# Kernel tuning notes

Hardware: AMD Instinct MI355X
Metric: run time of the kernel (lower is better)

## Reference

```python
import jax, jax.numpy as jnp
import numpy as np

NUM_BOXES = 512
NUM_COORDS = 200000
C = 128
MAX_SELECTED = 262144  # static pad size for the ragged output
P_INSIDE = 0.002       # expected ~204.8k selected rows < MAX_SELECTED


def setup_inputs() -> dict:
    key = jax.random.key(0)
    k1, k2, k3 = jax.random.split(key, 3)
    coords = jax.random.randint(k1, (NUM_COORDS, 4), 0, 256, dtype=jnp.int32)
    features = jax.random.normal(k2, (NUM_COORDS, C), dtype=jnp.float32)
    is_inside = jax.random.uniform(k3, (NUM_BOXES, NUM_COORDS)) < P_INSIDE
    return {"coords": coords, "features": features, "is_inside": is_inside,
            "max_selected": MAX_SELECTED}


def reference(coords, features, is_inside, max_selected):
    # Faithful to select_coords/select_features, but WITHOUT materializing the
    # dense (num_boxes, num_coords, C) expand: compute flat nonzero indices of
    # the mask directly and gather once. Output is padded to a static size
    # (padded rows zeroed) since jax requires static shapes.
    num_boxes, num_coords = is_inside.shape
    total = num_boxes * num_coords
    flat_idx = jnp.nonzero(is_inside.ravel(), size=max_selected, fill_value=total)[0]
    valid = flat_idx < total                      # [K] pad mask
    safe = jnp.where(valid, flat_idx, 0)
    box_idx = (safe // num_coords).astype(jnp.int32)   # [K]
    coord_idx = safe % num_coords                       # [K]
    # select_features: features[None].expand(...)[is_inside]
    selected_features = jnp.where(valid[:, None], features[coord_idx], 0.0)  # [K, C]
    # select_coords: cat(coords[:, :-1] gathered, box index)
    sel_xyz = coords[coord_idx, :-1]                    # [K, 3]
    ext_coords = jnp.concatenate([sel_xyz, box_idx[:, None]], axis=-1)  # [K, 4]
    extended_coordinates = jnp.where(valid[:, None], ext_coords, 0)
    return extended_coordinates, selected_features
```

## Files before the change

### kernel.cpp

```cpp
#include <hip/hip_runtime.h>


#define BS  256
#define WPB 1024
#define DETB 32

__device__ __forceinline__ unsigned nzmask4(unsigned v){
  unsigned t = (v | ((v & 0x7f7f7f7fu) + 0x7f7f7f7fu)) & 0x80808080u;
  return ((t >> 7) & 1u) | ((t >> 14) & 2u) | ((t >> 21) & 4u) | ((t >> 28) & 8u);
}
__device__ __forceinline__ unsigned nzmask16(uint4 x){
  return nzmask4(x.x) | (nzmask4(x.y) << 4) | (nzmask4(x.z) << 8) | (nzmask4(x.w) << 12);
}

__global__ void detect_mode(const uchar4* p, int nvec, int* flags){
  int found = 0;
  for (int i = blockIdx.x*blockDim.x + threadIdx.x; i < nvec;
       i += gridDim.x*blockDim.x){
    uchar4 v = p[i];
    if (v.y) found = 1;
  }
  __shared__ int sh;
  if (threadIdx.x == 0) sh = 0;
  __syncthreads();
  if (found) atomicOr(&sh, 1);
  __syncthreads();
  if (threadIdx.x == 0) flags[blockIdx.x] = sh;
}

__global__ void pack_count(const void* data, const int* flags,
                           long long totalElems, int wordsTotal,
                           unsigned* maskOut, int* counts){
  __shared__ int modeSh;
  if (threadIdx.x == 0){
    int f = 0;
    for (int i = 0; i < DETB; ++i) f |= flags[i];
    modeSh = f;
  }
  __syncthreads();
  const bool byteMode = (modeSh != 0);
  const int tid = threadIdx.x;
  int cnt = 0;
  const int wBase = blockIdx.x * WPB;
  if (byteMode){
    const uint4* d = (const uint4*)data;
    const unsigned char* p8 = (const unsigned char*)data;
    for (int i = tid; i < WPB; i += BS){
      const int w = wBase + i;
      if (w >= wordsTotal) break;
      const long long e0 = (long long)w << 5;
      unsigned m;
      if (e0 + 31 < totalElems){
        uint4 a = d[2*w], b = d[2*w+1];
        m = nzmask16(a) | (nzmask16(b) << 16);
      } else {
        m = 0;
        for (int b = 0; b < 32 && e0 + b < totalElems; ++b)
          if (p8[e0 + b]) m |= (1u << b);
      }
      maskOut[w] = m;
      cnt += __popc(m);
    }
  } else {
    const uint4* d = (const uint4*)data;
    const unsigned* p32 = (const unsigned*)data;
    for (int i = tid; i < WPB; i += BS){
      const int w = wBase + i;
      if (w >= wordsTotal) break;
      const long long e0 = (long long)w << 5;
      unsigned m = 0;
      if (e0 + 31 < totalElems){
        #pragma unroll
        for (int k = 0; k < 8; ++k){
          uint4 x = d[8*(long long)w + k];
          m |= ((unsigned)(x.x!=0) << (4*k)) | ((unsigned)(x.y!=0) << (4*k+1)) |
               ((unsigned)(x.z!=0) << (4*k+2)) | ((unsigned)(x.w!=0) << (4*k+3));
        }
      } else {
        for (int b = 0; b < 32 && e0 + b < totalElems; ++b)
          if (p32[e0 + b]) m |= (1u << b);
      }
      maskOut[w] = m;
      cnt += __popc(m);
    }
  }
  const int lane = tid & 63, wid = tid >> 6;
  for (int off = 32; off > 0; off >>= 1) cnt += __shfl_down(cnt, off, 64);
  __shared__ int wsum[BS/64];
  if (lane == 0) wsum[wid] = cnt;
  __syncthreads();
  if (tid == 0){
    int s = 0;
    for (int w = 0; w < BS/64; ++w) s += wsum[w];
    counts[blockIdx.x] = s;
  }
}

__global__ void scan_kernel(const int* counts, int* offsets, int* totalOut, int nb){
  const int tid = threadIdx.x;
  const int per = (nb + BS - 1)/BS;
  const int base = tid*per;
  int vals[16];
  int sum = 0;
  for (int k = 0; k < per; ++k){
    int idx = base + k;
    int c = (idx < nb) ? counts[idx] : 0;
    vals[k] = sum; sum += c;
  }
  int incl = sum;
  const int lane = tid & 63, wid = tid >> 6;
  for (int off = 1; off < 64; off <<= 1){
    int t = __shfl_up(incl, off, 64);
    if (lane >= off) incl += t;
  }
  __shared__ int wsum[BS/64];
  if (lane == 63) wsum[wid] = incl;
  __syncthreads();
  int wbase = 0;
  for (int w = 0; w < wid; ++w) wbase += wsum[w];
  const int excl = wbase + incl - sum;
  for (int k = 0; k < per; ++k){
    int idx = base + k;
    if (idx < nb) offsets[idx] = excl + vals[k];
  }
  if (tid == BS-1){
    int t = 0;
    for (int w = 0; w < BS/64; ++w) t += wsum[w];
    *totalOut = t;
  }
}

__global__ void emit_kernel(const unsigned* mask, const int* offsets,
                            int wordsTotal, int max_sel, int* outIdx){
  const int tid = threadIdx.x;
  const int lane = tid & 63, wid = tid >> 6;
  const int wBase = blockIdx.x * WPB;
  int running = offsets[blockIdx.x];
  __shared__ int wsum[BS/64];
  const int iters = WPB / BS;
  for (int it = 0; it < iters; ++it){
    const int w = wBase + it*BS + tid;
    unsigned m = (w < wordsTotal) ? mask[w] : 0u;
    const int cnt = __popc(m);
    int incl = cnt;
    for (int off = 1; off < 64; off <<= 1){
      int t = __shfl_up(incl, off, 64);
      if (lane >= off) incl += t;
    }
    if (lane == 63) wsum[wid] = incl;
    __syncthreads();
    int wbase = 0;
    for (int ww = 0; ww < wid; ++ww) wbase += wsum[ww];
    int iterTotal = 0;
    for (int ww = 0; ww < BS/64; ++ww) iterTotal += wsum[ww];
    int pos = running + wbase + incl - cnt;
    if (m){
      const long long e0 = (long long)w << 5;
      unsigned mm = m;
      while (mm){
        const int b = __ffs(mm) - 1;
        mm &= mm - 1;
        if (pos < max_sel) outIdx[pos] = (int)(e0 + b);
        ++pos;
      }
    }
    running += iterTotal;
    __syncthreads();
  }
}

__global__ void gather_kernel(const int* selIdx, const int* totalPtr,
                              const int4* coords, const float4* feat,
                              int num_coords, int c4, int max_sel,
                              float4* outExt, float4* outFeat){
  const int lane = threadIdx.x & 31;
  const int rowsPerBlock = blockDim.x >> 5;
  const int r = blockIdx.x*rowsPerBlock + (threadIdx.x >> 5);
  if (r >= max_sel) return;
  int total = *totalPtr;
  if (total > max_sel) total = max_sel;
  if (r < total){
    const int flat = selIdx[r];
    const unsigned box = (unsigned)flat / (unsigned)num_coords;
    const int ci = flat - (int)box*num_coords;
    const float4* src = feat + (long long)ci*c4;
    float4* dst = outFeat + (long long)r*c4;
    for (int c = lane; c < c4; c += 32) dst[c] = src[c];
    if (lane == 0){
      int4 cc = coords[ci];
      outExt[r] = make_float4((float)cc.x, (float)cc.y, (float)cc.z, (float)box);
    }
  } else {
    const float4 z = make_float4(0.f, 0.f, 0.f, 0.f);
    float4* dst = outFeat + (long long)r*c4;
    for (int c = lane; c < c4; c += 32) dst[c] = z;
    if (lane == 0) outExt[r] = z;
  }
}

extern "C" void kernel_launch(void* const* d_in, const int* in_sizes, int n_in,
                              void* d_out, int out_size, void* d_ws, size_t ws_size,
                              hipStream_t stream){
  const int*   coords   = (const int*)d_in[0];
  const float* features = (const float*)d_in[1];
  const void*  inside   = d_in[2];

  const int num_coords = in_sizes[0] / 4;
  const int C          = in_sizes[1] / num_coords;
  const int c4         = C / 4;
  const long long totalElems = (long long)in_sizes[2];
  const int max_sel    = out_size / (4 + C);

  const int wordsTotal = (int)((totalElems + 31) / 32);
  const int NBP        = (wordsTotal + WPB - 1) / WPB;

  int* ws      = (int*)d_ws;
  int* flags   = ws;
  int* total   = ws + DETB;
  int* counts  = ws + DETB + 1;
  int* offsets = counts + NBP;
  int* selIdx  = offsets + NBP;
  unsigned* maskBuf = (unsigned*)(selIdx + max_sel);

  hipLaunchKernelGGL(detect_mode, dim3(DETB), dim3(BS), 0, stream,
                     (const uchar4*)inside, 65536 , flags);
  hipLaunchKernelGGL(pack_count, dim3(NBP), dim3(BS), 0, stream,
                     inside, flags, totalElems, wordsTotal, maskBuf, counts);
  hipLaunchKernelGGL(scan_kernel, dim3(1), dim3(BS), 0, stream,
                     counts, offsets, total, NBP);
  hipLaunchKernelGGL(emit_kernel, dim3(NBP), dim3(BS), 0, stream,
                     maskBuf, offsets, wordsTotal, max_sel, selIdx);
  const int rowsPerBlock = BS / 32;
  const int gblocks = (max_sel + rowsPerBlock - 1) / rowsPerBlock;
  hipLaunchKernelGGL(gather_kernel, dim3(gblocks), dim3(BS), 0, stream,
                     selIdx, total, (const int4*)coords, (const float4*)features,
                     num_coords, c4, max_sel,
                     (float4*)d_out,
                     (float4*)((float*)d_out + (long long)max_sel*4));
}
```

Measured before the change: 670.9 us.

## Make pack/emit per-wavefront chunks, add nontemporal loads/stores, grid-stride gather

Pack and emit kernels now give each 64-lane wavefront its own chunk of mask words, which removes the block-level shared-memory reductions and __syncthreads. Mask reads and gather output writes use nontemporal loads and stores to avoid polluting cache during streaming. The gather kernel becomes a fixed 2048-block grid-stride loop. The scan now handles four times more chunk counts (vals array raised to 64), so the single-block scan does more serial work per thread.

```diff
diff --git a/kernel.cpp b/kernel.cpp
--- a/kernel.cpp
+++ b/kernel.cpp
@@ -1,15 +1,20 @@
 #include <hip/hip_runtime.h>
 
 
-#define BS  256
-#define WPB 1024
+#define BS   256
+#define WPW  256
+#define CPB  4
 #define DETB 32
+
+using uint4v  = __attribute__((ext_vector_type(4))) unsigned int;
+using int4v   = __attribute__((ext_vector_type(4))) int;
+using float4v = __attribute__((ext_vector_type(4))) float;
 
 __device__ __forceinline__ unsigned nzmask4(unsigned v){
   unsigned t = (v | ((v & 0x7f7f7f7fu) + 0x7f7f7f7fu)) & 0x80808080u;
   return ((t >> 7) & 1u) | ((t >> 14) & 2u) | ((t >> 21) & 4u) | ((t >> 28) & 8u);
 }
-__device__ __forceinline__ unsigned nzmask16(uint4 x){
+__device__ __forceinline__ unsigned nzmask16(uint4v x){
   return nzmask4(x.x) | (nzmask4(x.y) << 4) | (nzmask4(x.z) << 8) | (nzmask4(x.w) << 12);
 }
 
@@ -29,7 +34,7 @@
 }
 
 __global__ void pack_count(const void* data, const int* flags,
-                           long long totalElems, int wordsTotal,
+                           long long totalElems, int wordsTotal, int nchunks,
                            unsigned* maskOut, int* counts){
   __shared__ int modeSh;
   if (threadIdx.x == 0){
@@ -39,68 +44,66 @@
   }
   __syncthreads();
   const bool byteMode = (modeSh != 0);
-  const int tid = threadIdx.x;
+  const int lane  = threadIdx.x & 63;
+  const int wv    = threadIdx.x >> 6;
+  const int chunk = blockIdx.x*CPB + wv;
+  if (chunk >= nchunks) return;
+  const int wBase = chunk * WPW;
   int cnt = 0;
-  const int wBase = blockIdx.x * WPB;
   if (byteMode){
-    const uint4* d = (const uint4*)data;
+    const uint4v* d = (const uint4v*)data;
     const unsigned char* p8 = (const unsigned char*)data;
-    for (int i = tid; i < WPB; i += BS){
-      const int w = wBase + i;
-      if (w >= wordsTotal) break;
+    #pragma unroll
+    for (int it = 0; it < WPW/64; ++it){
+      const int w = wBase + it*64 + lane;
+      if (w >= wordsTotal) continue;
       const long long e0 = (long long)w << 5;
       unsigned m;
       if (e0 + 31 < totalElems){
-        uint4 a = d[2*w], b = d[2*w+1];
+        uint4v a = __builtin_nontemporal_load(d + 2*(long long)w);
+        uint4v b = __builtin_nontemporal_load(d + 2*(long long)w + 1);
         m = nzmask16(a) | (nzmask16(b) << 16);
       } else {
         m = 0;
-        for (int b = 0; b < 32 && e0 + b < totalElems; ++b)
-          if (p8[e0 + b]) m |= (1u << b);
+        for (int bb = 0; bb < 32 && e0 + bb < totalElems; ++bb)
+          if (p8[e0 + bb]) m |= (1u << bb);
       }
       maskOut[w] = m;
       cnt += __popc(m);
     }
   } else {
-    const uint4* d = (const uint4*)data;
+    const uint4v* d = (const uint4v*)data;
     const unsigned* p32 = (const unsigned*)data;
-    for (int i = tid; i < WPB; i += BS){
-      const int w = wBase + i;
-      if (w >= wordsTotal) break;
+    #pragma unroll
+    for (int it = 0; it < WPW/64; ++it){
+      const int w = wBase + it*64 + lane;
+      if (w >= wordsTotal) continue;
       const long long e0 = (long long)w << 5;
       unsigned m = 0;
       if (e0 + 31 < totalElems){
         #pragma unroll
         for (int k = 0; k < 8; ++k){
-          uint4 x = d[8*(long long)w + k];
-          m |= ((unsigned)(x.x!=0) << (4*k)) | ((unsigned)(x.y!=0) << (4*k+1)) |
+          uint4v x = __builtin_nontemporal_load(d + 8*(long long)w + k);
+          m |= ((unsigned)(x.x!=0) << (4*k))   | ((unsigned)(x.y!=0) << (4*k+1)) |
                ((unsigned)(x.z!=0) << (4*k+2)) | ((unsigned)(x.w!=0) << (4*k+3));
         }
       } else {
-        for (int b = 0; b < 32 && e0 + b < totalElems; ++b)
-          if (p32[e0 + b]) m |= (1u << b);
+        for (int bb = 0; bb < 32 && e0 + bb < totalElems; ++bb)
+          if (p32[e0 + bb]) m |= (1u << bb);
       }
       maskOut[w] = m;
       cnt += __popc(m);
     }
   }
-  const int lane = tid & 63, wid = tid >> 6;
   for (int off = 32; off > 0; off >>= 1) cnt += __shfl_down(cnt, off, 64);
-  __shared__ int wsum[BS/64];
-  if (lane == 0) wsum[wid] = cnt;
-  __syncthreads();
-  if (tid == 0){
-    int s = 0;
-    for (int w = 0; w < BS/64; ++w) s += wsum[w];
-    counts[blockIdx.x] = s;
-  }
+  if (lane == 0) counts[chunk] = cnt;
 }
 
 __global__ void scan_kernel(const int* counts, int* offsets, int* totalOut, int nb){
   const int tid = threadIdx.x;
   const int per = (nb + BS - 1)/BS;
   const int base = tid*per;
-  int vals[16];
+  int vals[64];
   int sum = 0;
   for (int k = 0; k < per; ++k){
     int idx = base + k;
@@ -131,15 +134,16 @@
 }
 
 __global__ void emit_kernel(const unsigned* mask, const int* offsets,
-                            int wordsTotal, int max_sel, int* outIdx){
-  const int tid = threadIdx.x;
-  const int lane = tid & 63, wid = tid >> 6;
-  const int wBase = blockIdx.x * WPB;
-  int running = offsets[blockIdx.x];
-  __shared__ int wsum[BS/64];
-  const int iters = WPB / BS;
-  for (int it = 0; it < iters; ++it){
-    const int w = wBase + it*BS + tid;
+                            int wordsTotal, int nchunks, int max_sel, int* outIdx){
+  const int lane  = threadIdx.x & 63;
+  const int wv    = threadIdx.x >> 6;
+  const int chunk = blockIdx.x*CPB + wv;
+  if (chunk >= nchunks) return;
+  int running = offsets[chunk];
+  const int wBase = chunk * WPW;
+  #pragma unroll
+  for (int it = 0; it < WPW/64; ++it){
+    const int w = wBase + it*64 + lane;
     unsigned m = (w < wordsTotal) ? mask[w] : 0u;
     const int cnt = __popc(m);
     int incl = cnt;
@@ -147,54 +151,47 @@
       int t = __shfl_up(incl, off, 64);
       if (lane >= off) incl += t;
     }
-    if (lane == 63) wsum[wid] = incl;
-    __syncthreads();
-    int wbase = 0;
-    for (int ww = 0; ww < wid; ++ww) wbase += wsum[ww];
-    int iterTotal = 0;
-    for (int ww = 0; ww < BS/64; ++ww) iterTotal += wsum[ww];
-    int pos = running + wbase + incl - cnt;
-    if (m){
-      const long long e0 = (long long)w << 5;
-      unsigned mm = m;
-      while (mm){
-        const int b = __ffs(mm) - 1;
-        mm &= mm - 1;
-        if (pos < max_sel) outIdx[pos] = (int)(e0 + b);
-        ++pos;
-      }
-    }
-    running += iterTotal;
-    __syncthreads();
+    int pos = running + incl - cnt;
+    const long long e0 = (long long)w << 5;
+    while (m){
+      const int b = __ffs(m) - 1;
+      m &= m - 1;
+      if (pos < max_sel) outIdx[pos] = (int)(e0 + b);
+      ++pos;
+    }
+    running += __shfl(incl, 63, 64);
   }
 }
 
 __global__ void gather_kernel(const int* selIdx, const int* totalPtr,
-                              const int4* coords, const float4* feat,
+                              const int4v* coords, const float4v* feat,
                               int num_coords, int c4, int max_sel,
-                              float4* outExt, float4* outFeat){
-  const int lane = threadIdx.x & 31;
-  const int rowsPerBlock = blockDim.x >> 5;
-  const int r = blockIdx.x*rowsPerBlock + (threadIdx.x >> 5);
-  if (r >= max_sel) return;
+                              float4v* outExt, float4v* outFeat){
   int total = *totalPtr;
   if (total > max_sel) total = max_sel;
-  if (r < total){
-    const int flat = selIdx[r];
-    const unsigned box = (unsigned)flat / (unsigned)num_coords;
-    const int ci = flat - (int)box*num_coords;
-    const float4* src = feat + (long long)ci*c4;
-    float4* dst = outFeat + (long long)r*c4;
-    for (int c = lane; c < c4; c += 32) dst[c] = src[c];
-    if (lane == 0){
-      int4 cc = coords[ci];
-      outExt[r] = make_float4((float)cc.x, (float)cc.y, (float)cc.z, (float)box);
-    }
-  } else {
-    const float4 z = make_float4(0.f, 0.f, 0.f, 0.f);
-    float4* dst = outFeat + (long long)r*c4;
-    for (int c = lane; c < c4; c += 32) dst[c] = z;
-    if (lane == 0) outExt[r] = z;
+  const int lane   = threadIdx.x & 31;
+  const int warp   = (blockIdx.x*blockDim.x + threadIdx.x) >> 5;
+  const int nwarps = (gridDim.x*blockDim.x) >> 5;
+  for (int r = warp; r < max_sel; r += nwarps){
+    float4v* dst = outFeat + (long long)r*c4;
+    if (r < total){
+      const int flat = selIdx[r];
+      const unsigned box = (unsigned)flat / (unsigned)num_coords;
+      const int ci = flat - (int)box*num_coords;
+      const float4v* src = feat + (long long)ci*c4;
+      for (int c = lane; c < c4; c += 32)
+        __builtin_nontemporal_store(src[c], dst + c);
+      if (lane == 0){
+        int4v cc = coords[ci];
+        float4v e = { (float)cc.x, (float)cc.y, (float)cc.z, (float)box };
+        __builtin_nontemporal_store(e, outExt + r);
+      }
+    } else {
+      const float4v z = { 0.f, 0.f, 0.f, 0.f };
+      for (int c = lane; c < c4; c += 32)
+        __builtin_nontemporal_store(z, dst + c);
+      if (lane == 0) __builtin_nontemporal_store(z, outExt + r);
+    }
   }
 }
 
@@ -212,29 +209,29 @@
   const int max_sel    = out_size / (4 + C);
 
   const int wordsTotal = (int)((totalElems + 31) / 32);
-  const int NBP        = (wordsTotal + WPB - 1) / WPB;
+  const int nchunks    = (wordsTotal + WPW - 1) / WPW;
+  const int nblocks    = (nchunks + CPB - 1) / CPB;
 
   int* ws      = (int*)d_ws;
   int* flags   = ws;
   int* total   = ws + DETB;
   int* counts  = ws + DETB + 1;
-  int* offsets = counts + NBP;
-  int* selIdx  = offsets + NBP;
+  int* offsets = counts + nchunks;
+  int* selIdx  = offsets + nchunks;
   unsigned* maskBuf = (unsigned*)(selIdx + max_sel);
 
   hipLaunchKernelGGL(detect_mode, dim3(DETB), dim3(BS), 0, stream,
                      (const uchar4*)inside, 65536 , flags);
-  hipLaunchKernelGGL(pack_count, dim3(NBP), dim3(BS), 0, stream,
-                     inside, flags, totalElems, wordsTotal, maskBuf, counts);
+  hipLaunchKernelGGL(pack_count, dim3(nblocks), dim3(BS), 0, stream,
+                     inside, flags, totalElems, wordsTotal, nchunks,
+                     maskBuf, counts);
   hipLaunchKernelGGL(scan_kernel, dim3(1), dim3(BS), 0, stream,
-                     counts, offsets, total, NBP);
-  hipLaunchKernelGGL(emit_kernel, dim3(NBP), dim3(BS), 0, stream,
-                     maskBuf, offsets, wordsTotal, max_sel, selIdx);
-  const int rowsPerBlock = BS / 32;
-  const int gblocks = (max_sel + rowsPerBlock - 1) / rowsPerBlock;
-  hipLaunchKernelGGL(gather_kernel, dim3(gblocks), dim3(BS), 0, stream,
-                     selIdx, total, (const int4*)coords, (const float4*)features,
+                     counts, offsets, total, nchunks);
+  hipLaunchKernelGGL(emit_kernel, dim3(nblocks), dim3(BS), 0, stream,
+                     maskBuf, offsets, wordsTotal, nchunks, max_sel, selIdx);
+  hipLaunchKernelGGL(gather_kernel, dim3(2048), dim3(BS), 0, stream,
+                     selIdx, total, (const int4v*)coords, (const float4v*)features,
                      num_coords, c4, max_sel,
-                     (float4*)d_out,
-                     (float4*)((float*)d_out + (long long)max_sel*4));
-}
+                     (float4v*)d_out,
+                     (float4v*)((float*)d_out + (long long)max_sel*4));
+}
```

Measured after the change: 771.0 us. 1.15x slower.
